# Kernel tuning notes

Measured on AMD Instinct MI355X. Metric: run time of the kernel, lower is better.

## Reference

```python
import jax, jax.numpy as jnp
import numpy as np
from jax import lax

LN_EPS = 1e-5

def _conv1d(h, w, b):
    # h: [N, L, Cin], w: [Cout, Cin, K] (torch Conv1d layout), padding=1
    out = lax.conv_general_dilated(h, w, window_strides=(1,), padding=[(1, 1)],
                                   dimension_numbers=("NWC", "OIW", "NWC"))
    return out + b

def _layer_norm(h, g, b):
    m = jnp.mean(h, axis=-1, keepdims=True)
    v = jnp.mean((h - m) ** 2, axis=-1, keepdims=True)
    return (h - m) * lax.rsqrt(v + LN_EPS) * g + b

def setup_inputs() -> dict:
    key = jax.random.key(0)
    ks = jax.random.split(key, 8)
    N, L, D, F = 32, 512, 384, 256
    return {
        "x": jax.random.normal(ks[0], (N, L, D), jnp.float32),
        "conv1_w": jax.random.normal(ks[1], (F, D, 3), jnp.float32) * 0.05,
        "conv1_b": jnp.zeros((F,), jnp.float32),
        "ln1_g": jnp.ones((F,), jnp.float32),
        "ln1_b": jnp.zeros((F,), jnp.float32),
        "conv2_w": jax.random.normal(ks[2], (F, F, 3), jnp.float32) * 0.05,
        "conv2_b": jnp.zeros((F,), jnp.float32),
        "ln2_g": jnp.ones((F,), jnp.float32),
        "ln2_b": jnp.zeros((F,), jnp.float32),
        "lin_w": jax.random.normal(ks[3], (F,), jnp.float32) * 0.05,
        "lin_b": jnp.zeros((), jnp.float32),
        "target": jax.random.randint(ks[4], (N, L), 0, 8, dtype=jnp.int32),
        "mel_max_length": 2048,
    }

def reference(x, conv1_w, conv1_b, ln1_g, ln1_b, conv2_w, conv2_b, ln2_g, ln2_b,
              lin_w, lin_b, target, mel_max_length):
    # Duration predictor (dropout is identity at inference)
    h = jax.nn.relu(_layer_norm(_conv1d(x, conv1_w, conv1_b), ln1_g, ln1_b))
    h = jax.nn.relu(_layer_norm(_conv1d(h, conv2_w, conv2_b), ln2_g, ln2_b))
    duration_predictor_output = jnp.einsum("nlf,f->nl", h, lin_w) + lin_b  # [N, L]

    # LR: frame t copies phoneme j iff cumsum(dur)[:j] <= t < cumsum(dur)[:j+1]
    # (equivalent to the one-hot alignment matmul, padded to mel_max_length)
    N, L, D = x.shape
    T = mel_max_length
    cums = jnp.cumsum(target, axis=-1)                      # [N, L]
    frames = jnp.arange(T, dtype=cums.dtype)                # [T]
    idx = jax.vmap(lambda c: jnp.searchsorted(c, frames, side="right"))(cums)  # [N, T]
    valid = frames[None, :] < cums[:, -1:]                  # frames beyond total are zero
    gathered = jnp.take_along_axis(x, jnp.clip(idx, 0, L - 1)[:, :, None], axis=1)
    output = gathered * valid[:, :, None].astype(x.dtype)   # [N, T, D]
    return output, duration_predictor_output
```

## Files before the change

kernel.cpp:

```cpp
#include <hip/hip_runtime.h>
#include <hip/hip_bf16.h>

typedef unsigned short u16;
typedef short s8v __attribute__((ext_vector_type(8)));
typedef float f4v __attribute__((ext_vector_type(4)));
typedef u16 u16x8 __attribute__((ext_vector_type(8)));

static __device__ __forceinline__ u16 f2bf(float v) {
    __hip_bfloat16 h = __float2bfloat16(v);
    return *(u16*)&h;
}

__global__ __launch_bounds__(256) void gather_prep_kernel(
    const float* __restrict__ x,
    const int*   __restrict__ target,
    const float* __restrict__ w1,
    const float* __restrict__ w2,
    u16* __restrict__ Wt1,
    u16* __restrict__ Wt2,
    float* __restrict__ out0)
{
    __shared__ int c[512];
    __shared__ int ridx[64];
    const int b = blockIdx.x, tid = threadIdx.x;

    if (b >= 1024) {
        if (b < 2176) {
            const int K = 1152, DIN = 384;
            int e = (b - 1024) * 256 + tid;
            int f = e / K;
            int rem = e - f * K;
            int kc = rem / DIN;
            int d = rem - kc * DIN;
            Wt1[e] = f2bf(w1[f * K + d * 3 + kc]);
        } else {
            const int K = 768, DIN = 256;
            int e = (b - 2176) * 256 + tid;
            int f = e / K;
            int rem = e - f * K;
            int kc = rem / DIN;
            int d = rem - kc * DIN;
            Wt2[e] = f2bf(w2[f * K + d * 3 + kc]);
        }
        return;
    }

    const int n = b >> 5, sub = b & 31;
    c[tid]       = target[n * 512 + tid];
    c[tid + 256] = target[n * 512 + 256 + tid];
    __syncthreads();
    for (int off = 1; off < 512; off <<= 1) {
        int v0 = (tid       >= off) ? c[tid       - off] : 0;
        int v1 = (tid + 256 >= off) ? c[tid + 256 - off] : 0;
        __syncthreads();
        c[tid]       += v0;
        c[tid + 256] += v1;
        __syncthreads();
    }
    const int total = c[511];
    if (tid < 64) {
        int t = sub * 64 + tid;
        int lo = 0, hi = 512;
        while (lo < hi) {
            int mid = (lo + hi) >> 1;
            if (c[mid] <= t) lo = mid + 1; else hi = mid;
        }
        ridx[tid] = (t < total) ? min(lo, 511) : -1;
    }
    __syncthreads();

    const size_t xbase = (size_t)(n << 9) * 384;
    const size_t obase = ((size_t)(n << 11) + sub * 64) * 384;
    #pragma unroll 4
    for (int it = 0; it < 12; ++it) {
        int u  = tid + it * 256;
        int j  = u % 48;
        int rl = u / 48;
        int ie = ridx[rl];
        f4v v0 = {0.f, 0.f, 0.f, 0.f}, v1 = v0;
        if (ie >= 0) {
            const float* src = &x[xbase + (size_t)ie * 384];
            v0 = *(const f4v*)&src[j * 4];
            v1 = *(const f4v*)&src[(j + 48) * 4];
        }
        float* dst = &out0[obase + (size_t)rl * 384];
        __builtin_nontemporal_store(v0, (f4v*)&dst[j * 4]);
        __builtin_nontemporal_store(v1, (f4v*)&dst[(j + 48) * 4]);
    }
}

__global__ __launch_bounds__(256, 2) void fused_conv_kernel(
    const float* __restrict__ x,
    const u16* __restrict__ Wt1,
    const u16* __restrict__ Wt2,
    const float* __restrict__ cb1, const float* __restrict__ g1,
    const float* __restrict__ bb1,
    const float* __restrict__ cb2, const float* __restrict__ g2,
    const float* __restrict__ bb2,
    const float* __restrict__ lw, const float* __restrict__ lbp,
    float* __restrict__ dpo)
{
    __shared__ __align__(128) char LDS[79872];
    float* redS = (float*)(LDS + 77824);
    float* redQ = (float*)(LDS + 78592);
    float* redP = (float*)(LDS + 79360);

    const int tid  = threadIdx.x;
    const int lane = tid & 63, wc = tid >> 6;
    const int lr = lane & 15, q4 = lane >> 4;
    const int sb = (blockIdx.x & 7) * 64 + (blockIdx.x >> 3);
    const int m0 = sb * 32;
    const int n  = m0 >> 9, l0 = m0 & 511;

    const int b_r    = tid >> 3;
    const int b_slot = (tid & 7) ^ (b_r & 7);
    int boff[4];
    #pragma unroll
    for (int ni = 0; ni < 4; ni++) boff[ni] = (64 * wc + 16 * ni + lr) * 128;
    const int slot0 = ((q4)     ^ (lr & 7)) << 4;
    const int slot1 = ((q4 | 4) ^ (lr & 7)) << 4;

    f4v acc[3][4];
    #pragma unroll
    for (int mi = 0; mi < 3; mi++)
        #pragma unroll
        for (int ni = 0; ni < 4; ni++) acc[mi][ni] = {0.f, 0.f, 0.f, 0.f};

    auto stage1 = [&](int buf, int t) {
        const int k0 = t * 64;
        const int kc = k0 / 384;
        const int d0 = k0 - kc * 384;
        char* As = LDS + 65536 + buf * 6144;
        for (int u = tid; u < 384; u += 256) {
            int ar = u >> 3;
            int aslot = (u & 7) ^ (ar & 7);
            int lp = l0 - 8 + ar + kc - 1;
            f4v v0 = {0.f, 0.f, 0.f, 0.f}, v1 = v0;
            if (lp >= 0 && lp < 512) {
                const float* src = x + ((size_t)((n << 9) + lp)) * 384 + d0 + (u & 7) * 8;
                v0 = *(const f4v*)src;
                v1 = *(const f4v*)(src + 4);
            }
            u16x8 r;
            #pragma unroll
            for (int jj = 0; jj < 4; jj++) { r[jj] = f2bf(v0[jj]); r[4 + jj] = f2bf(v1[jj]); }
            *(u16x8*)(As + ar * 128 + aslot * 16) = r;
        }
        const u16* bsrc = Wt1 + (size_t)b_r * 1152 + k0 + b_slot * 8;
        #pragma unroll
        for (int q = 0; q < 8; q++) {
            __builtin_amdgcn_global_load_lds(
                (const __attribute__((address_space(1))) void*)(bsrc + (size_t)q * 32 * 1152),
                (__attribute__((address_space(3))) void*)(LDS + buf * 32768 + q * 4096 + tid * 16),
                16, 0, 0);
        }
    };

    auto compute1 = [&](int buf) {
        char* As = LDS + 65536 + buf * 6144;
        char* Bs = LDS + buf * 32768;
        #pragma unroll
        for (int kk = 0; kk < 2; kk++) {
            const int sl = kk ? slot1 : slot0;
            s8v a0 = *(const s8v*)(As + (lr) * 128 + sl);
            s8v a1 = *(const s8v*)(As + (16 + lr) * 128 + sl);
            s8v a2 = *(const s8v*)(As + (32 + lr) * 128 + sl);
            s8v b0 = *(const s8v*)(Bs + boff[0] + sl);
            s8v b1 = *(const s8v*)(Bs + boff[1] + sl);
            s8v b2 = *(const s8v*)(Bs + boff[2] + sl);
            s8v b3 = *(const s8v*)(Bs + boff[3] + sl);
            acc[0][0] = __builtin_amdgcn_mfma_f32_16x16x32_bf16(a0, b0, acc[0][0], 0, 0, 0);
            acc[0][1] = __builtin_amdgcn_mfma_f32_16x16x32_bf16(a0, b1, acc[0][1], 0, 0, 0);
            acc[0][2] = __builtin_amdgcn_mfma_f32_16x16x32_bf16(a0, b2, acc[0][2], 0, 0, 0);
            acc[0][3] = __builtin_amdgcn_mfma_f32_16x16x32_bf16(a0, b3, acc[0][3], 0, 0, 0);
            acc[1][0] = __builtin_amdgcn_mfma_f32_16x16x32_bf16(a1, b0, acc[1][0], 0, 0, 0);
            acc[1][1] = __builtin_amdgcn_mfma_f32_16x16x32_bf16(a1, b1, acc[1][1], 0, 0, 0);
            acc[1][2] = __builtin_amdgcn_mfma_f32_16x16x32_bf16(a1, b2, acc[1][2], 0, 0, 0);
            acc[1][3] = __builtin_amdgcn_mfma_f32_16x16x32_bf16(a1, b3, acc[1][3], 0, 0, 0);
            acc[2][0] = __builtin_amdgcn_mfma_f32_16x16x32_bf16(a2, b0, acc[2][0], 0, 0, 0);
            acc[2][1] = __builtin_amdgcn_mfma_f32_16x16x32_bf16(a2, b1, acc[2][1], 0, 0, 0);
            acc[2][2] = __builtin_amdgcn_mfma_f32_16x16x32_bf16(a2, b2, acc[2][2], 0, 0, 0);
            acc[2][3] = __builtin_amdgcn_mfma_f32_16x16x32_bf16(a2, b3, acc[2][3], 0, 0, 0);
        }
    };

    stage1(0, 0);
    __syncthreads();
    int cur = 0;
    for (int t = 0; t < 18; ++t) {
        if (t + 1 < 18) stage1(cur ^ 1, t + 1);
        compute1(cur);
        __syncthreads();
        cur ^= 1;
    }

    int col[4];
    float cbv[4], gv[4], bbv[4];
    #pragma unroll
    for (int ni = 0; ni < 4; ni++) {
        col[ni] = 64 * wc + 16 * ni + lr;
        cbv[ni] = cb1[col[ni]]; gv[ni] = g1[col[ni]]; bbv[ni] = bb1[col[ni]];
    }

    #pragma unroll
    for (int mi = 0; mi < 3; mi++)
        #pragma unroll
        for (int reg = 0; reg < 4; reg++) {
            float s = 0.f, q = 0.f;
            #pragma unroll
            for (int ni = 0; ni < 4; ni++) {
                float v = acc[mi][ni][reg] + cbv[ni];
                s += v; q += v * v;
            }
            #pragma unroll
            for (int msk = 1; msk < 16; msk <<= 1) {
                s += __shfl_xor(s, msk);
                q += __shfl_xor(q, msk);
            }
            if (lr == 0) {
                int rl = 16 * mi + 4 * q4 + reg;
                redS[rl * 4 + wc] = s;
                redQ[rl * 4 + wc] = q;
            }
        }
    __syncthreads();

    #pragma unroll
    for (int mi = 0; mi < 3; mi++)
        #pragma unroll
        for (int reg = 0; reg < 4; reg++) {
            int rl = 16 * mi + 4 * q4 + reg;
            int h  = rl - 7;
            if (h >= 0 && h < 34) {
                float4 ps = *(float4*)&redS[rl * 4];
                float4 pq = *(float4*)&redQ[rl * 4];
                float mean = (ps.x + ps.y + ps.z + ps.w) * (1.f / 256.f);
                float var  = (pq.x + pq.y + pq.z + pq.w) * (1.f / 256.f) - mean * mean;
                float rs   = rsqrtf(var + 1e-5f);
                int l = l0 - 8 + rl;
                bool lv = (l >= 0 && l < 512);
                #pragma unroll
                for (int ni = 0; ni < 4; ni++) {
                    float v = acc[mi][ni][reg] + cbv[ni];
                    float o = lv ? fmaxf(0.f, (v - mean) * rs * gv[ni] + bbv[ni]) : 0.f;
                    int slot = (col[ni] >> 3) ^ (h & 7);
                    *(u16*)(LDS + h * 512 + slot * 16 + (col[ni] & 7) * 2) = f2bf(o);
                }
            }
        }

    f4v acc2[2][4];
    #pragma unroll
    for (int mi = 0; mi < 2; mi++)
        #pragma unroll
        for (int ni = 0; ni < 4; ni++) acc2[mi][ni] = {0.f, 0.f, 0.f, 0.f};

    for (int t2 = 0; t2 < 12; ++t2) {
        __syncthreads();
        const int k0 = t2 * 64;
        const u16* bsrc = Wt2 + (size_t)b_r * 768 + k0 + b_slot * 8;
        #pragma unroll
        for (int q = 0; q < 8; q++) {
            __builtin_amdgcn_global_load_lds(
                (const __attribute__((address_space(1))) void*)(bsrc + (size_t)q * 32 * 768),
                (__attribute__((address_space(3))) void*)(LDS + 32768 + q * 4096 + tid * 16),
                16, 0, 0);
        }
        __syncthreads();

        const int kc2   = t2 >> 2;
        const int sbase = 8 * (t2 & 3);
        #pragma unroll
        for (int kk = 0; kk < 2; kk++) {
            const int sl = kk ? slot1 : slot0;
            char* Bs = LDS + 32768;
            s8v b0 = *(const s8v*)(Bs + boff[0] + sl);
            s8v b1 = *(const s8v*)(Bs + boff[1] + sl);
            s8v b2 = *(const s8v*)(Bs + boff[2] + sl);
            s8v b3 = *(const s8v*)(Bs + boff[3] + sl);
            s8v a0, a1;
            {
                int h = lr + kc2;
                int s = sbase + 4 * kk + q4;
                a0 = *(const s8v*)(LDS + h * 512 + ((s ^ (h & 7)) << 4));
                h = 16 + lr + kc2;
                a1 = *(const s8v*)(LDS + h * 512 + ((s ^ (h & 7)) << 4));
            }
            acc2[0][0] = __builtin_amdgcn_mfma_f32_16x16x32_bf16(a0, b0, acc2[0][0], 0, 0, 0);
            acc2[0][1] = __builtin_amdgcn_mfma_f32_16x16x32_bf16(a0, b1, acc2[0][1], 0, 0, 0);
            acc2[0][2] = __builtin_amdgcn_mfma_f32_16x16x32_bf16(a0, b2, acc2[0][2], 0, 0, 0);
            acc2[0][3] = __builtin_amdgcn_mfma_f32_16x16x32_bf16(a0, b3, acc2[0][3], 0, 0, 0);
            acc2[1][0] = __builtin_amdgcn_mfma_f32_16x16x32_bf16(a1, b0, acc2[1][0], 0, 0, 0);
            acc2[1][1] = __builtin_amdgcn_mfma_f32_16x16x32_bf16(a1, b1, acc2[1][1], 0, 0, 0);
            acc2[1][2] = __builtin_amdgcn_mfma_f32_16x16x32_bf16(a1, b2, acc2[1][2], 0, 0, 0);
            acc2[1][3] = __builtin_amdgcn_mfma_f32_16x16x32_bf16(a1, b3, acc2[1][3], 0, 0, 0);
        }
    }

    float cbv2[4], gv2[4], bbv2[4], lwv[4];
    #pragma unroll
    for (int ni = 0; ni < 4; ni++) {
        cbv2[ni] = cb2[col[ni]]; gv2[ni] = g2[col[ni]]; bbv2[ni] = bb2[col[ni]];
        lwv[ni]  = lw[col[ni]];
    }

    float sv[2][4], sq[2][4];
    #pragma unroll
    for (int mi = 0; mi < 2; mi++)
        #pragma unroll
        for (int reg = 0; reg < 4; reg++) {
            float s = 0.f, q = 0.f;
            #pragma unroll
            for (int ni = 0; ni < 4; ni++) {
                float v = acc2[mi][ni][reg] + cbv2[ni];
                s += v; q += v * v;
            }
            #pragma unroll
            for (int msk = 1; msk < 16; msk <<= 1) {
                s += __shfl_xor(s, msk);
                q += __shfl_xor(q, msk);
            }
            sv[mi][reg] = s; sq[mi][reg] = q;
        }
    __syncthreads();
    if (lr == 0) {
        #pragma unroll
        for (int mi = 0; mi < 2; mi++)
            #pragma unroll
            for (int reg = 0; reg < 4; reg++) {
                int rl = 16 * mi + 4 * q4 + reg;
                redS[rl * 4 + wc] = sv[mi][reg];
                redQ[rl * 4 + wc] = sq[mi][reg];
            }
    }
    __syncthreads();

    float pp[2][4];
    #pragma unroll
    for (int mi = 0; mi < 2; mi++)
        #pragma unroll
        for (int reg = 0; reg < 4; reg++) {
            int rl = 16 * mi + 4 * q4 + reg;
            float4 ps = *(float4*)&redS[rl * 4];
            float4 pq = *(float4*)&redQ[rl * 4];
            float mean = (ps.x + ps.y + ps.z + ps.w) * (1.f / 256.f);
            float var  = (pq.x + pq.y + pq.z + pq.w) * (1.f / 256.f) - mean * mean;
            float rs   = rsqrtf(var + 1e-5f);
            float p = 0.f;
            #pragma unroll
            for (int ni = 0; ni < 4; ni++) {
                float v = acc2[mi][ni][reg] + cbv2[ni];
                float o = fmaxf(0.f, (v - mean) * rs * gv2[ni] + bbv2[ni]);
                p += o * lwv[ni];
            }
            #pragma unroll
            for (int msk = 1; msk < 16; msk <<= 1) p += __shfl_xor(p, msk);
            pp[mi][reg] = p;
        }
    if (lr == 0) {
        #pragma unroll
        for (int mi = 0; mi < 2; mi++)
            #pragma unroll
            for (int reg = 0; reg < 4; reg++) {
                int rl = 16 * mi + 4 * q4 + reg;
                redP[rl * 4 + wc] = pp[mi][reg];
            }
    }
    __syncthreads();
    if (tid < 32) {
        float4 p4 = *(float4*)&redP[tid * 4];
        dpo[m0 + tid] = p4.x + p4.y + p4.z + p4.w + lbp[0];
    }
}

extern "C" void kernel_launch(void* const* d_in, const int* in_sizes, int n_in,
                              void* d_out, int out_size, void* d_ws, size_t ws_size,
                              hipStream_t stream) {
    const float* x   = (const float*)d_in[0];
    const float* w1  = (const float*)d_in[1];
    const float* b1  = (const float*)d_in[2];
    const float* g1  = (const float*)d_in[3];
    const float* bb1 = (const float*)d_in[4];
    const float* w2  = (const float*)d_in[5];
    const float* b2  = (const float*)d_in[6];
    const float* g2  = (const float*)d_in[7];
    const float* bb2 = (const float*)d_in[8];
    const float* lw  = (const float*)d_in[9];
    const float* lb  = (const float*)d_in[10];
    const int* target = (const int*)d_in[11];

    char* wsb = (char*)d_ws;
    u16*  Wt1 = (u16*)wsb;
    u16*  Wt2 = (u16*)(wsb + 589824);

    float* out0 = (float*)d_out;
    float* dpo  = out0 + (size_t)32 * 2048 * 384;

    gather_prep_kernel<<<2944, 256, 0, stream>>>(
        x, target, w1, w2, Wt1, Wt2, out0);

    fused_conv_kernel<<<512, 256, 0, stream>>>(
        x, Wt1, Wt2, b1, g1, bb1, b2, g2, bb2, lw, lb, dpo);
}
```

Baseline: 70.10 us.

## Stage full bf16 input window in LDS once, drop conv1 double buffering

The conv1 stage now loads the block's whole 50-row input window from global memory once, converting it to bf16 into a swizzled LDS region. The three conv taps then read shifted rows from that region instead of reloading and reconverting x for every k-tile. The conv1 weight staging becomes single-buffered, with two barriers per iteration and one shared B region reused by conv2, which shrinks LDS use. In exchange, the weight loads no longer overlap MFMA compute, so load latency is exposed on every iteration.

```diff
diff --git a/kernel.cpp b/kernel.cpp
--- a/kernel.cpp
+++ b/kernel.cpp
@@ -100,10 +100,11 @@
     const float* __restrict__ lw, const float* __restrict__ lbp,
     float* __restrict__ dpo)
 {
-    __shared__ __align__(128) char LDS[79872];
-    float* redS = (float*)(LDS + 77824);
-    float* redQ = (float*)(LDS + 78592);
-    float* redP = (float*)(LDS + 79360);
+    __shared__ __align__(128) char LDS[73216];
+    char* Bs    = LDS + 38400;
+    float* redS = (float*)(LDS + 71168);
+    float* redQ = (float*)(LDS + 71936);
+    float* redP = (float*)(LDS + 72704);
 
     const int tid  = threadIdx.x;
     const int lane = tid & 63, wc = tid >> 6;
@@ -120,51 +121,55 @@
     const int slot0 = ((q4)     ^ (lr & 7)) << 4;
     const int slot1 = ((q4 | 4) ^ (lr & 7)) << 4;
 
+    for (int u = tid; u < 2400; u += 256) {
+        int j = u / 48, s = u - j * 48;
+        int lp = l0 - 9 + j;
+        f4v v0 = {0.f, 0.f, 0.f, 0.f}, v1 = v0;
+        if (lp >= 0 && lp < 512) {
+            const float* src = x + ((size_t)((n << 9) + lp)) * 384 + s * 8;
+            v0 = *(const f4v*)src;
+            v1 = *(const f4v*)(src + 4);
+        }
+        u16x8 r;
+        #pragma unroll
+        for (int jj = 0; jj < 4; jj++) { r[jj] = f2bf(v0[jj]); r[4 + jj] = f2bf(v1[jj]); }
+        int ss = (s & ~7) | ((s & 7) ^ (j & 7));
+        *(u16x8*)(LDS + j * 768 + ss * 16) = r;
+    }
+
+    auto xwread = [&](int j, int s) -> s8v {
+        int ss = (s & ~7) | ((s & 7) ^ (j & 7));
+        return *(const s8v*)(LDS + j * 768 + (ss << 4));
+    };
+
     f4v acc[3][4];
     #pragma unroll
     for (int mi = 0; mi < 3; mi++)
         #pragma unroll
         for (int ni = 0; ni < 4; ni++) acc[mi][ni] = {0.f, 0.f, 0.f, 0.f};
 
-    auto stage1 = [&](int buf, int t) {
+    for (int t = 0; t < 18; ++t) {
+        __syncthreads();
         const int k0 = t * 64;
-        const int kc = k0 / 384;
-        const int d0 = k0 - kc * 384;
-        char* As = LDS + 65536 + buf * 6144;
-        for (int u = tid; u < 384; u += 256) {
-            int ar = u >> 3;
-            int aslot = (u & 7) ^ (ar & 7);
-            int lp = l0 - 8 + ar + kc - 1;
-            f4v v0 = {0.f, 0.f, 0.f, 0.f}, v1 = v0;
-            if (lp >= 0 && lp < 512) {
-                const float* src = x + ((size_t)((n << 9) + lp)) * 384 + d0 + (u & 7) * 8;
-                v0 = *(const f4v*)src;
-                v1 = *(const f4v*)(src + 4);
-            }
-            u16x8 r;
-            #pragma unroll
-            for (int jj = 0; jj < 4; jj++) { r[jj] = f2bf(v0[jj]); r[4 + jj] = f2bf(v1[jj]); }
-            *(u16x8*)(As + ar * 128 + aslot * 16) = r;
-        }
         const u16* bsrc = Wt1 + (size_t)b_r * 1152 + k0 + b_slot * 8;
         #pragma unroll
         for (int q = 0; q < 8; q++) {
             __builtin_amdgcn_global_load_lds(
                 (const __attribute__((address_space(1))) void*)(bsrc + (size_t)q * 32 * 1152),
-                (__attribute__((address_space(3))) void*)(LDS + buf * 32768 + q * 4096 + tid * 16),
+                (__attribute__((address_space(3))) void*)(Bs + q * 4096 + tid * 16),
                 16, 0, 0);
         }
-    };
-
-    auto compute1 = [&](int buf) {
-        char* As = LDS + 65536 + buf * 6144;
-        char* Bs = LDS + buf * 32768;
+        __syncthreads();
+
+        const int kc = k0 / 384;
+        const int s0 = (k0 - kc * 384) >> 3;
         #pragma unroll
         for (int kk = 0; kk < 2; kk++) {
             const int sl = kk ? slot1 : slot0;
-            s8v a0 = *(const s8v*)(As + (lr) * 128 + sl);
-            s8v a1 = *(const s8v*)(As + (16 + lr) * 128 + sl);
-            s8v a2 = *(const s8v*)(As + (32 + lr) * 128 + sl);
+            const int s  = s0 + 4 * kk + q4;
+            s8v a0 = xwread(lr + kc,      s);
+            s8v a1 = xwread(16 + lr + kc, s);
+            s8v a2 = xwread(32 + lr + kc, s);
             s8v b0 = *(const s8v*)(Bs + boff[0] + sl);
             s8v b1 = *(const s8v*)(Bs + boff[1] + sl);
             s8v b2 = *(const s8v*)(Bs + boff[2] + sl);
@@ -182,16 +187,6 @@
             acc[2][2] = __builtin_amdgcn_mfma_f32_16x16x32_bf16(a2, b2, acc[2][2], 0, 0, 0);
             acc[2][3] = __builtin_amdgcn_mfma_f32_16x16x32_bf16(a2, b3, acc[2][3], 0, 0, 0);
         }
-    };
-
-    stage1(0, 0);
-    __syncthreads();
-    int cur = 0;
-    for (int t = 0; t < 18; ++t) {
-        if (t + 1 < 18) stage1(cur ^ 1, t + 1);
-        compute1(cur);
-        __syncthreads();
-        cur ^= 1;
     }
 
     int col[4];
@@ -263,7 +258,7 @@
         for (int q = 0; q < 8; q++) {
             __builtin_amdgcn_global_load_lds(
                 (const __attribute__((address_space(1))) void*)(bsrc + (size_t)q * 32 * 768),
-                (__attribute__((address_space(3))) void*)(LDS + 32768 + q * 4096 + tid * 16),
+                (__attribute__((address_space(3))) void*)(Bs + q * 4096 + tid * 16),
                 16, 0, 0);
         }
         __syncthreads();
@@ -273,7 +268,6 @@
         #pragma unroll
         for (int kk = 0; kk < 2; kk++) {
             const int sl = kk ? slot1 : slot0;
-            char* Bs = LDS + 32768;
             s8v b0 = *(const s8v*)(Bs + boff[0] + sl);
             s8v b1 = *(const s8v*)(Bs + boff[1] + sl);
             s8v b2 = *(const s8v*)(Bs + boff[2] + sl);
```

Measured after the change: 67.65 us. -3.5%, faster.
